# Performance work log

Measured on AMD Instinct MI355X. Metric: run time of the kernel, lower is better.

The kernel has to match this reference:

```python
import jax, jax.numpy as jnp
import numpy as np

B, L, E, H = 2, 2048, 1024, 16
D = E // H  # head dim = 64


def setup_inputs() -> dict:
    key = jax.random.key(0)
    ks = jax.random.split(key, 10)
    s = 0.02
    return {
        "xt": jax.random.normal(ks[0], (B, L, E), jnp.float32),
        "xs": jax.random.normal(ks[1], (B, L, E), jnp.float32),
        "Wt": jax.random.normal(ks[2], (E, 3 * E), jnp.float32) * s,  # t_attn weight (x @ Wt)
        "bt": jnp.zeros((3 * E,), jnp.float32),
        "Ws": jax.random.normal(ks[3], (E, 2 * E), jnp.float32) * s,  # s_attn weight
        "bs": jnp.zeros((2 * E,), jnp.float32),
        "Wc": jax.random.normal(ks[4], (E, E), jnp.float32) * s,      # c_proj weight
        "bc": jnp.zeros((E,), jnp.float32),
        "lam_ts": jnp.ones((1,), jnp.float32),
        "lam_st": jnp.ones((1,), jnp.float32),
        "lam_ss": jnp.ones((1,), jnp.float32),
    }


def _heads(x):
    # (B, L, E) -> (B, H, L, D)
    return x.reshape(B, L, H, D).transpose(0, 2, 1, 3)


def reference(xt, xs, Wt, bt, Ws, bs, Wc, bc, lam_ts, lam_st, lam_ss):
    qt, kt, vt = jnp.split(xt @ Wt + bt, 3, axis=2)
    qs, ks = jnp.split(xs @ Ws + bs, 2, axis=2)
    qt, kt, vt, qs, ks = map(_heads, (qt, kt, vt, qs, ks))

    # 4-way disentangled scores; fuse the 4 matmuls into 2 by combining keys:
    # qt@kt^T + lam_ts*qt@ks^T = qt @ (kt + lam_ts*ks)^T
    # lam_st*qs@kt^T + lam_ss*qs@ks^T = qs @ (lam_st*kt + lam_ss*ks)^T
    k1 = kt + lam_ts[0] * ks
    k2 = lam_st[0] * kt + lam_ss[0] * ks
    att = (jnp.einsum('bhqd,bhkd->bhqk', qt, k1)
           + jnp.einsum('bhqd,bhkd->bhqk', qs, k2)) * (1.0 / np.sqrt(D))
    att = jax.nn.softmax(att, axis=-1)
    y = jnp.einsum('bhqk,bhkd->bhqd', att, vt)  # (B, H, L, D)
    y = y.transpose(0, 2, 1, 3).reshape(B, L, E)
    return y @ Wc + bc
```

## Files before the change

### kernel.cpp

```cpp
#include <hip/hip_runtime.h>
#include <math.h>

#define LQ 2048
#define EQ 1024
#define M_ROWS 4096
#define BH 32

typedef _Float16 f16x8 __attribute__((ext_vector_type(8)));
typedef _Float16 f16x4 __attribute__((ext_vector_type(4)));
typedef _Float16 f16x2 __attribute__((ext_vector_type(2)));
typedef float f32x4 __attribute__((ext_vector_type(4)));
typedef float f32x16 __attribute__((ext_vector_type(16)));

#define QSCALE 0.1803368801111204f
#define DEFER_THR 8.0f

__device__ __forceinline__ void async_ld16(const _Float16* g, _Float16* l) {
  __builtin_amdgcn_global_load_lds(
      (const __attribute__((address_space(1))) unsigned int*)g,
      (__attribute__((address_space(3))) unsigned int*)l, 16, 0, 0);
}

__global__ __launch_bounds__(256) void prep(
    const float* __restrict__ xt, const float* __restrict__ xs,
    const float* __restrict__ Wt, const float* __restrict__ Ws,
    const float* __restrict__ Wc,
    _Float16* __restrict__ xt16, _Float16* __restrict__ xs16,
    _Float16* __restrict__ WtT, _Float16* __restrict__ WsT,
    _Float16* __restrict__ WcT) {
  int gb = blockIdx.x;
  if (gb < 4096) {
    int i = gb * 256 + threadIdx.x;
    const float* s; _Float16* d; size_t off;
    if (i < 524288) { s = xt; d = xt16; off = (size_t)i * 8; }
    else            { s = xs; d = xs16; off = (size_t)(i - 524288) * 8; }
    float4 a = *(const float4*)&s[off];
    float4 b = *(const float4*)&s[off + 4];
    f16x8 h;
    h[0] = (_Float16)a.x; h[1] = (_Float16)a.y; h[2] = (_Float16)a.z; h[3] = (_Float16)a.w;
    h[4] = (_Float16)b.x; h[5] = (_Float16)b.y; h[6] = (_Float16)b.z; h[7] = (_Float16)b.w;
    *(f16x8*)&d[off] = h;
  } else {
    __shared__ float T[32][65];
    int tb = gb - 4096;
    int c0 = (tb % 96) * 64;
    int k0 = (tb / 96) * 32;
    const float* W; _Float16* D; int Nw, cl;
    if (c0 < 3072)      { W = Wt; D = WtT; Nw = 3072; cl = c0; }
    else if (c0 < 5120) { W = Ws; D = WsT; Nw = 2048; cl = c0 - 3072; }
    else                { W = Wc; D = WcT; Nw = 1024; cl = c0 - 5120; }
    const int tid = threadIdx.x;
#pragma unroll
    for (int p = 0; p < 4; ++p) {
      int idx = tid + p * 256;
      int row = idx >> 5;
      int c2 = (idx & 31) * 2;
      float2 v = *(const float2*)&W[(size_t)(k0 + row) * Nw + cl + c2];
      T[row][c2] = v.x;
      T[row][c2 + 1] = v.y;
    }
    __syncthreads();
#pragma unroll
    for (int p = 0; p < 4; ++p) {
      int idx = tid + p * 256;
      int col = idx >> 4;
      int k2 = (idx & 15) * 2;
      f16x2 h2;
      h2[0] = (_Float16)T[k2][col];
      h2[1] = (_Float16)T[k2 + 1][col];
      *(f16x2*)&D[(size_t)(cl + col) * 1024 + k0 + k2] = h2;
    }
  }
}

__global__ __launch_bounds__(256, 3) void proj_gemm(
    const _Float16* __restrict__ xt16, const _Float16* __restrict__ xs16,
    const _Float16* __restrict__ WtT, const _Float16* __restrict__ WsT,
    const float* __restrict__ bt, const float* __restrict__ bs,
    _Float16* __restrict__ q16, _Float16* __restrict__ k16,
    _Float16* __restrict__ v16) {
  __shared__ _Float16 LS[128 * 128];
  _Float16* Al0 = LS;
  _Float16* Bl0 = LS + 4096;
  _Float16* Al1 = LS + 8192;
  _Float16* Bl1 = LS + 12288;

  const int tid = threadIdx.x;
  const int w = tid >> 6;
  const int lane = tid & 63;
  const int quad = lane >> 4;
  const int l15 = lane & 15;
  const int wm = w >> 1, wn = w & 1;

  const int wg = blockIdx.y * 16 + blockIdx.x;
  const int swz = (wg & 7) * 160 + (wg >> 3);
  const int bx = swz & 15;
  const int by = swz >> 4;
  const int n0 = bx * 128;

  const _Float16* Ab;
  const _Float16* Bb;
  const float* bias;
  int m0, bsel = 0, branch;
  if (by < 32) {
    branch = 0; Ab = xt16; Bb = WtT; bias = bt; m0 = by * 128;
  } else if (by < 48) {
    branch = 1;
    int by2 = by - 32;
    bsel = by2 >> 3;
    m0 = (by2 & 7) * 128;
    Ab = WtT + (size_t)2048 * 1024;
    Bb = xt16 + (size_t)bsel * 2048 * 1024;
    bias = bt;
  } else {
    branch = 2; Ab = xs16; Bb = WsT; bias = bs; m0 = (by - 48) * 128;
  }

  const int srow = lane >> 2;
  const int schunk = ((lane & 3) ^ ((lane >> 3) & 3)) * 8;
  const int key = (l15 >> 1) & 3;

  f32x4 acc[4][4];
#pragma unroll
  for (int mb = 0; mb < 4; ++mb)
#pragma unroll
    for (int nb = 0; nb < 4; ++nb) acc[mb][nb] = (f32x4){0.f, 0.f, 0.f, 0.f};

  auto dma = [&](int kt, _Float16* Al, _Float16* Bl) {
#pragma unroll
    for (int i = 0; i < 2; ++i) {
      int rt = w * 32 + i * 16;
      async_ld16(&Ab[(size_t)(m0 + rt + srow) * 1024 + kt + schunk], &Al[rt * 32]);
      async_ld16(&Bb[(size_t)(n0 + rt + srow) * 1024 + kt + schunk], &Bl[rt * 32]);
    }
  };

  auto comp = [&](const _Float16* Al, const _Float16* Bl) {
    f16x8 af[4], bf[4];
    const int pc = (quad ^ key) * 8;
#pragma unroll
    for (int mb = 0; mb < 4; ++mb)
      af[mb] = *(const f16x8*)&Al[(wm * 64 + mb * 16 + l15) * 32 + pc];
#pragma unroll
    for (int nb = 0; nb < 4; ++nb)
      bf[nb] = *(const f16x8*)&Bl[(wn * 64 + nb * 16 + l15) * 32 + pc];
#pragma unroll
    for (int mb = 0; mb < 4; ++mb)
#pragma unroll
      for (int nb = 0; nb < 4; ++nb)
        acc[mb][nb] = __builtin_amdgcn_mfma_f32_16x16x32_f16(bf[nb], af[mb], acc[mb][nb], 0, 0, 0);
  };

  dma(0, Al0, Bl0);
  for (int kt = 0; kt < 1024; kt += 64) {
    __syncthreads();
    dma(kt + 32, Al1, Bl1);
    comp(Al0, Bl0);
    __syncthreads();
    if (kt + 64 < 1024) dma(kt + 64, Al0, Bl0);
    comp(Al1, Bl1);
  }

  __syncthreads();
#pragma unroll
  for (int mb = 0; mb < 4; ++mb) {
    const int rowL = wm * 64 + mb * 16 + l15;
    const int rx = (rowL & 7) << 3;
    float rbias = 0.f;
    if (branch == 1) rbias = bias[2048 + m0 + rowL];
#pragma unroll
    for (int nb = 0; nb < 4; ++nb) {
      const int colL = wn * 64 + nb * 16 + quad * 4;
      f16x4 o4;
      if (branch == 1) {
#pragma unroll
        for (int r = 0; r < 4; ++r) o4[r] = (_Float16)(acc[mb][nb][r] + rbias);
      } else {
        const float4 bv4 = *(const float4*)&bias[n0 + colL];
        o4[0] = (_Float16)(acc[mb][nb][0] + bv4.x);
        o4[1] = (_Float16)(acc[mb][nb][1] + bv4.y);
        o4[2] = (_Float16)(acc[mb][nb][2] + bv4.z);
        o4[3] = (_Float16)(acc[mb][nb][3] + bv4.w);
      }
      *(f16x4*)&LS[rowL * 128 + (colL ^ rx)] = o4;
    }
  }
  __syncthreads();

  const int g = tid & 15;
  const int c8 = g * 8;
#pragma unroll
  for (int p = 0; p < 8; ++p) {
    const int r = p * 16 + (tid >> 4);
    f16x8 v8 = *(const f16x8*)&LS[r * 128 + (c8 ^ ((r & 7) << 3))];
    if (branch == 1) {
      *(f16x8*)&v16[(size_t)(bsel * 1024 + m0 + r) * 2048 + n0 + c8] = v8;
    } else {
      const int grow = m0 + r;
      const int col = n0 + c8;
      const int bb = grow >> 11, ll = grow & 2047;
      const int which = col >> 10, e = col & 1023;
      const int hh = e >> 6, dd = e & 63;
      _Float16* dst = which ? k16 : q16;
      const int off = (branch == 0) ? 0 : 64;
      *(f16x8*)&dst[((size_t)(bb * 16 + hh) * 2048 + ll) * 128 + off + dd] = v8;
    }
  }
}

__global__ __launch_bounds__(256, 3) void cproj_gemm(
    const _Float16* __restrict__ A, const _Float16* __restrict__ Bm,
    const float* __restrict__ bias, float* __restrict__ outf) {
  __shared__ _Float16 Al0[128 * 32];
  __shared__ _Float16 Bl0[64 * 32];
  __shared__ _Float16 Al1[128 * 32];
  __shared__ _Float16 Bl1[64 * 32];

  const int tid = threadIdx.x;
  const int w = tid >> 6;
  const int lane = tid & 63;
  const int quad = lane >> 4;
  const int l15 = lane & 15;
  const int wm = w >> 1, wn = w & 1;
  const int m0 = blockIdx.y * 128;
  const int n0 = blockIdx.x * 64;

  const int srow = lane >> 2;
  const int schunk = ((lane & 3) ^ ((lane >> 3) & 3)) * 8;

  f32x4 acc[4][2];
#pragma unroll
  for (int mb = 0; mb < 4; ++mb)
#pragma unroll
    for (int nb = 0; nb < 2; ++nb) acc[mb][nb] = (f32x4){0.f, 0.f, 0.f, 0.f};

  const int key = (l15 >> 1) & 3;

  auto dma = [&](int kt, _Float16* Al, _Float16* Bl) {
#pragma unroll
    for (int i = 0; i < 2; ++i) {
      int rt = w * 32 + i * 16;
      async_ld16(&A[(size_t)(m0 + rt + srow) * 1024 + kt + schunk], &Al[rt * 32]);
    }
    int rtb = w * 16;
    async_ld16(&Bm[(size_t)(n0 + rtb + srow) * 1024 + kt + schunk], &Bl[rtb * 32]);
  };

  auto comp = [&](const _Float16* Al, const _Float16* Bl) {
    f16x8 af[4], bf[2];
    const int pc = (quad ^ key) * 8;
#pragma unroll
    for (int mb = 0; mb < 4; ++mb)
      af[mb] = *(const f16x8*)&Al[(wm * 64 + mb * 16 + l15) * 32 + pc];
#pragma unroll
    for (int nb = 0; nb < 2; ++nb)
      bf[nb] = *(const f16x8*)&Bl[(wn * 32 + nb * 16 + l15) * 32 + pc];
#pragma unroll
    for (int mb = 0; mb < 4; ++mb)
#pragma unroll
      for (int nb = 0; nb < 2; ++nb)
        acc[mb][nb] = __builtin_amdgcn_mfma_f32_16x16x32_f16(bf[nb], af[mb], acc[mb][nb], 0, 0, 0);
  };

  dma(0, Al0, Bl0);
  for (int kt = 0; kt < 1024; kt += 64) {
    __syncthreads();
    dma(kt + 32, Al1, Bl1);
    comp(Al0, Bl0);
    __syncthreads();
    if (kt + 64 < 1024) dma(kt + 64, Al0, Bl0);
    comp(Al1, Bl1);
  }

#pragma unroll
  for (int nb = 0; nb < 2; ++nb) {
    const int col0 = n0 + wn * 32 + nb * 16 + quad * 4;
    const float4 bv4 = *(const float4*)&bias[col0];
#pragma unroll
    for (int mb = 0; mb < 4; ++mb) {
      int row = m0 + wm * 64 + mb * 16 + l15;
      float4 o4;
      o4.x = acc[mb][nb][0] + bv4.x;
      o4.y = acc[mb][nb][1] + bv4.y;
      o4.z = acc[mb][nb][2] + bv4.z;
      o4.w = acc[mb][nb][3] + bv4.w;
      *(float4*)&outf[(size_t)row * 1024 + col0] = o4;
    }
  }
}

__global__ __launch_bounds__(256, 2) void flash_attn_mfma(
    const _Float16* __restrict__ qcat, const _Float16* __restrict__ kcat,
    const _Float16* __restrict__ vT, _Float16* __restrict__ y,
    const float* __restrict__ lam_ts, const float* __restrict__ lam_st,
    const float* __restrict__ lam_ss) {
  const int bh = blockIdx.y;
  const int qt0 = blockIdx.x * 128;
  const int b = bh >> 4, h = bh & 15;
  const _Float16* Qg = qcat + (size_t)bh * LQ * 128;
  const _Float16* Kg = kcat + (size_t)bh * LQ * 128;
  const _Float16* Vg = vT + (size_t)bh * 64 * LQ;

  __shared__ _Float16 K0s[64 * 128];
  __shared__ _Float16 K1s[64 * 128];
  __shared__ _Float16 V0s[64 * 64];
  __shared__ _Float16 V1s[64 * 64];
  __shared__ _Float16 V2s[64 * 64];
  __shared__ _Float16 V3s[64 * 64];

  const int tid = threadIdx.x;
  const int w = tid >> 6;
  const int lane = tid & 63;
  const int half = lane >> 5;
  const int l31 = lane & 31;

  const float lts = lam_ts[0], lst = lam_st[0], lss = lam_ss[0];

  f16x8 qf[8];
#pragma unroll
  for (int db = 0; db < 4; ++db) {
    const _Float16* qp = &Qg[(size_t)(qt0 + w * 32 + l31) * 128 + db * 16 + half * 8];
    f16x8 a = *(const f16x8*)qp;
    f16x8 bq = *(const f16x8*)(qp + 64);
#pragma unroll
    for (int e = 0; e < 8; ++e) {
      float fa = (float)a[e], fb = (float)bq[e];
      qf[db][e]     = (_Float16)(QSCALE * (fa + lst * fb));
      qf[db + 4][e] = (_Float16)(QSCALE * (lts * fa + lss * fb));
    }
  }

  float m_i = -INFINITY;
  float l_i = 0.f;
  f32x16 O[2];
#pragma unroll
  for (int nt = 0; nt < 2; ++nt)
#pragma unroll
    for (int r = 0; r < 16; ++r) O[nt][r] = 0.f;

  auto dma_k = [&](int t, _Float16* Kd) {
#pragma unroll
    for (int a = 0; a < 4; ++a) {
      int row = w * 16 + a * 4 + (lane >> 4);
      int sc = (lane & 15) ^ (row & 7);
      async_ld16(&Kg[(size_t)(t + row) * 128 + sc * 8], &Kd[(w * 16 + a * 4) * 128]);
    }
  };
  auto dma_v = [&](int t, _Float16* Vd) {
#pragma unroll
    for (int a = 0; a < 2; ++a) {
      int row = w * 16 + a * 8 + (lane >> 3);
      int sc = (lane & 7) ^ (row & 7);
      async_ld16(&Vg[(size_t)row * LQ + t + sc * 8], &Vd[(w * 16 + a * 8) * 64]);
    }
  };

  auto qk = [&](const _Float16* Ks, f32x16* Sp) {
#pragma unroll
    for (int kb = 0; kb < 2; ++kb)
#pragma unroll
      for (int r = 0; r < 16; ++r) Sp[kb][r] = 0.f;
#pragma unroll
    for (int db = 0; db < 8; ++db) {
      const int pc = ((db * 2 + half) ^ (lane & 7)) * 8;
      f16x8 af0 = *(const f16x8*)&Ks[l31 * 128 + pc];
      f16x8 af1 = *(const f16x8*)&Ks[(32 + l31) * 128 + pc];
      Sp[0] = __builtin_amdgcn_mfma_f32_32x32x16_f16(af0, qf[db], Sp[0], 0, 0, 0);
      Sp[1] = __builtin_amdgcn_mfma_f32_32x32x16_f16(af1, qf[db], Sp[1], 0, 0, 0);
    }
  };

  auto softpv = [&](f32x16* S, const _Float16* Vs) {
    float mx = -INFINITY;
#pragma unroll
    for (int kb = 0; kb < 2; ++kb)
#pragma unroll
      for (int r = 0; r < 16; ++r) mx = fmaxf(mx, S[kb][r]);
    mx = fmaxf(mx, __shfl_xor(mx, 32));

    if (__any(mx > m_i + DEFER_THR)) {
      float m_new = fmaxf(m_i, mx);
      float alpha = __builtin_amdgcn_exp2f(m_i - m_new);
      l_i *= alpha;
#pragma unroll
      for (int nt = 0; nt < 2; ++nt)
#pragma unroll
        for (int r = 0; r < 16; ++r) O[nt][r] *= alpha;
      m_i = m_new;
    }

    float s = 0.f;
#pragma unroll
    for (int kb = 0; kb < 2; ++kb)
#pragma unroll
      for (int r = 0; r < 16; ++r) {
        float p = __builtin_amdgcn_exp2f(S[kb][r] - m_i);
        S[kb][r] = p;
        s += p;
      }
    s += __shfl_xor(s, 32);
    l_i += s;

#pragma unroll
    for (int kb = 0; kb < 2; ++kb) {
      unsigned pu[8];
#pragma unroll
      for (int i = 0; i < 8; ++i) {
        f16x2 t2;
        t2[0] = (_Float16)S[kb][2 * i];
        t2[1] = (_Float16)S[kb][2 * i + 1];
        pu[i] = __builtin_bit_cast(unsigned, t2);
      }
#pragma unroll
      for (int c = 0; c < 2; ++c) {
        unsigned u0 = pu[4 * c + 0], u1 = pu[4 * c + 1];
        unsigned u2 = pu[4 * c + 2], u3 = pu[4 * c + 3];
        asm("v_permlane32_swap_b32 %0, %1" : "+v"(u0), "+v"(u2));
        asm("v_permlane32_swap_b32 %0, %1" : "+v"(u1), "+v"(u3));
        union { unsigned u[4]; f16x8 v; } pb;
        pb.u[0] = u0; pb.u[1] = u1; pb.u[2] = u2; pb.u[3] = u3;
        const int kb2 = kb * 2 + c;
        f16x8 av[2];
#pragma unroll
        for (int nt = 0; nt < 2; ++nt) {
          int dim = nt * 32 + l31;
          int pc = ((kb2 * 2 + half) ^ (dim & 7)) * 8;
          av[nt] = *(const f16x8*)&Vs[dim * 64 + pc];
        }
#pragma unroll
        for (int nt = 0; nt < 2; ++nt)
          O[nt] = __builtin_amdgcn_mfma_f32_32x32x16_f16(av[nt], pb.v, O[nt], 0, 0, 0);
      }
    }
  };

  f32x16 Sa[2], Sb[2];

  dma_k(0, K0s);
  dma_v(0, V0s);
  __syncthreads();
  dma_k(64, K1s);
  dma_v(64, V1s);
  qk(K0s, Sb);

  for (int j = 0; j < 7; ++j) {
    const int t = j * 256 + 64;
    __syncthreads();
    dma_k(t + 64, K0s);  dma_v(t + 64, V2s);
    qk(K1s, Sa);  softpv(Sb, V0s);
    __syncthreads();
    dma_k(t + 128, K1s); dma_v(t + 128, V3s);
    qk(K0s, Sb);  softpv(Sa, V1s);
    __syncthreads();
    dma_k(t + 192, K0s); dma_v(t + 192, V0s);
    qk(K1s, Sa);  softpv(Sb, V2s);
    __syncthreads();
    dma_k(t + 256, K1s); dma_v(t + 256, V1s);
    qk(K0s, Sb);  softpv(Sa, V3s);
  }

  __syncthreads();
  dma_k(1920, K0s); dma_v(1920, V2s);
  qk(K1s, Sa);  softpv(Sb, V0s);
  __syncthreads();
  dma_k(1984, K1s); dma_v(1984, V3s);
  qk(K0s, Sb);  softpv(Sa, V1s);
  __syncthreads();
  qk(K1s, Sa);  softpv(Sb, V2s);
  softpv(Sa, V3s);

  float inv = 1.f / l_i;
  int qrow = qt0 + w * 32 + l31;
#pragma unroll
  for (int nt = 0; nt < 2; ++nt)
#pragma unroll
    for (int rg = 0; rg < 4; ++rg) {
      f16x4 o4;
#pragma unroll
      for (int i = 0; i < 4; ++i) o4[i] = (_Float16)(O[nt][rg * 4 + i] * inv);
      int dim = nt * 32 + rg * 8 + half * 4;
      *(f16x4*)&y[((size_t)b * LQ + qrow) * EQ + h * 64 + dim] = o4;
    }
}

extern "C" void kernel_launch(void* const* d_in, const int* in_sizes, int n_in,
                              void* d_out, int out_size, void* d_ws, size_t ws_size,
                              hipStream_t stream) {
  const float* xt = (const float*)d_in[0];
  const float* xs = (const float*)d_in[1];
  const float* Wt = (const float*)d_in[2];
  const float* bt = (const float*)d_in[3];
  const float* Ws = (const float*)d_in[4];
  const float* bs = (const float*)d_in[5];
  const float* Wc = (const float*)d_in[6];
  const float* bc = (const float*)d_in[7];
  const float* lam_ts = (const float*)d_in[8];
  const float* lam_st = (const float*)d_in[9];
  const float* lam_ss = (const float*)d_in[10];
  float* out = (float*)d_out;

  _Float16* w16 = (_Float16*)d_ws;
  _Float16* xt16 = w16;
  _Float16* xs16 = xt16 + 4194304;
  _Float16* WtT  = xs16 + 4194304;
  _Float16* WsT  = WtT + 3145728;
  _Float16* WcT  = WsT + 2097152;
  _Float16* qcat = WcT + 1048576;
  _Float16* kcat = qcat + 8388608;
  _Float16* vbufT = kcat + 8388608;
  _Float16* ybuf = vbufT + 4194304;

  prep<<<7168, 256, 0, stream>>>(xt, xs, Wt, Ws, Wc, xt16, xs16, WtT, WsT, WcT);
  proj_gemm<<<dim3(16, 80), 256, 0, stream>>>(
      xt16, xs16, WtT, WsT, bt, bs, qcat, kcat, vbufT);
  flash_attn_mfma<<<dim3(16, 32), 256, 0, stream>>>(
      qcat, kcat, vbufT, ybuf, lam_ts, lam_st, lam_ss);
  cproj_gemm<<<dim3(16, 32), 256, 0, stream>>>(ybuf, WcT, bc, out);
}
```

Baseline: 254.6 us.

## Halve flash attention query and KV tiles, use two-wave blocks

Shrinks the attention block from 4 waves and 128 queries to 2 waves and 64 queries, and the KV tile from 64 to 32 keys. The QK and PV lambdas are restructured for a single 32x32 score tile per wave, the LDS buffers and V swizzle are resized, and the grid doubles in x. The aim is more blocks for better CU load balance and lower LDS and register pressure. In exchange each K/V tile is reused by half as many queries, so global/L2 traffic and barrier count per unit of work roughly double.

```diff
diff --git a/kernel.cpp b/kernel.cpp
--- a/kernel.cpp
+++ b/kernel.cpp
@@ -289,24 +289,24 @@
   }
 }
 
-__global__ __launch_bounds__(256, 2) void flash_attn_mfma(
+__global__ __launch_bounds__(128, 2) void flash_attn_mfma(
     const _Float16* __restrict__ qcat, const _Float16* __restrict__ kcat,
     const _Float16* __restrict__ vT, _Float16* __restrict__ y,
     const float* __restrict__ lam_ts, const float* __restrict__ lam_st,
     const float* __restrict__ lam_ss) {
   const int bh = blockIdx.y;
-  const int qt0 = blockIdx.x * 128;
+  const int qt0 = blockIdx.x * 64;
   const int b = bh >> 4, h = bh & 15;
   const _Float16* Qg = qcat + (size_t)bh * LQ * 128;
   const _Float16* Kg = kcat + (size_t)bh * LQ * 128;
   const _Float16* Vg = vT + (size_t)bh * 64 * LQ;
 
-  __shared__ _Float16 K0s[64 * 128];
-  __shared__ _Float16 K1s[64 * 128];
-  __shared__ _Float16 V0s[64 * 64];
-  __shared__ _Float16 V1s[64 * 64];
-  __shared__ _Float16 V2s[64 * 64];
-  __shared__ _Float16 V3s[64 * 64];
+  __shared__ _Float16 K0s[32 * 128];
+  __shared__ _Float16 K1s[32 * 128];
+  __shared__ _Float16 V0s[64 * 32];
+  __shared__ _Float16 V1s[64 * 32];
+  __shared__ _Float16 V2s[64 * 32];
+  __shared__ _Float16 V3s[64 * 32];
 
   const int tid = threadIdx.x;
   const int w = tid >> 6;
@@ -349,33 +349,28 @@
   auto dma_v = [&](int t, _Float16* Vd) {
 #pragma unroll
     for (int a = 0; a < 2; ++a) {
-      int row = w * 16 + a * 8 + (lane >> 3);
-      int sc = (lane & 7) ^ (row & 7);
-      async_ld16(&Vg[(size_t)row * LQ + t + sc * 8], &Vd[(w * 16 + a * 8) * 64]);
+      int row = w * 32 + a * 16 + (lane >> 2);
+      int sc = (lane & 3) ^ (row & 3);
+      async_ld16(&Vg[(size_t)row * LQ + t + sc * 8], &Vd[(w * 32 + a * 16) * 32]);
     }
   };
 
   auto qk = [&](const _Float16* Ks, f32x16* Sp) {
 #pragma unroll
-    for (int kb = 0; kb < 2; ++kb)
-#pragma unroll
-      for (int r = 0; r < 16; ++r) Sp[kb][r] = 0.f;
+    for (int r = 0; r < 16; ++r) (*Sp)[r] = 0.f;
 #pragma unroll
     for (int db = 0; db < 8; ++db) {
       const int pc = ((db * 2 + half) ^ (lane & 7)) * 8;
       f16x8 af0 = *(const f16x8*)&Ks[l31 * 128 + pc];
-      f16x8 af1 = *(const f16x8*)&Ks[(32 + l31) * 128 + pc];
-      Sp[0] = __builtin_amdgcn_mfma_f32_32x32x16_f16(af0, qf[db], Sp[0], 0, 0, 0);
-      Sp[1] = __builtin_amdgcn_mfma_f32_32x32x16_f16(af1, qf[db], Sp[1], 0, 0, 0);
-    }
-  };
-
-  auto softpv = [&](f32x16* S, const _Float16* Vs) {
+      *Sp = __builtin_amdgcn_mfma_f32_32x32x16_f16(af0, qf[db], *Sp, 0, 0, 0);
+    }
+  };
+
+  auto softpv = [&](f32x16* Sp, const _Float16* Vs) {
+    f32x16& S = *Sp;
     float mx = -INFINITY;
 #pragma unroll
-    for (int kb = 0; kb < 2; ++kb)
-#pragma unroll
-      for (int r = 0; r < 16; ++r) mx = fmaxf(mx, S[kb][r]);
+    for (int r = 0; r < 16; ++r) mx = fmaxf(mx, S[r]);
     mx = fmaxf(mx, __shfl_xor(mx, 32));
 
     if (__any(mx > m_i + DEFER_THR)) {
@@ -391,83 +386,77 @@
 
     float s = 0.f;
 #pragma unroll
-    for (int kb = 0; kb < 2; ++kb)
-#pragma unroll
-      for (int r = 0; r < 16; ++r) {
-        float p = __builtin_amdgcn_exp2f(S[kb][r] - m_i);
-        S[kb][r] = p;
-        s += p;
-      }
+    for (int r = 0; r < 16; ++r) {
+      float p = __builtin_amdgcn_exp2f(S[r] - m_i);
+      S[r] = p;
+      s += p;
+    }
     s += __shfl_xor(s, 32);
     l_i += s;
 
-#pragma unroll
-    for (int kb = 0; kb < 2; ++kb) {
-      unsigned pu[8];
-#pragma unroll
-      for (int i = 0; i < 8; ++i) {
-        f16x2 t2;
-        t2[0] = (_Float16)S[kb][2 * i];
-        t2[1] = (_Float16)S[kb][2 * i + 1];
-        pu[i] = __builtin_bit_cast(unsigned, t2);
+    unsigned pu[8];
+#pragma unroll
+    for (int i = 0; i < 8; ++i) {
+      f16x2 t2;
+      t2[0] = (_Float16)S[2 * i];
+      t2[1] = (_Float16)S[2 * i + 1];
+      pu[i] = __builtin_bit_cast(unsigned, t2);
+    }
+#pragma unroll
+    for (int c = 0; c < 2; ++c) {
+      unsigned u0 = pu[4 * c + 0], u1 = pu[4 * c + 1];
+      unsigned u2 = pu[4 * c + 2], u3 = pu[4 * c + 3];
+      asm("v_permlane32_swap_b32 %0, %1" : "+v"(u0), "+v"(u2));
+      asm("v_permlane32_swap_b32 %0, %1" : "+v"(u1), "+v"(u3));
+      union { unsigned u[4]; f16x8 v; } pb;
+      pb.u[0] = u0; pb.u[1] = u1; pb.u[2] = u2; pb.u[3] = u3;
+      f16x8 av[2];
+#pragma unroll
+      for (int nt = 0; nt < 2; ++nt) {
+        int dim = nt * 32 + l31;
+        int pc = ((c * 2 + half) ^ (dim & 3)) * 8;
+        av[nt] = *(const f16x8*)&Vs[dim * 32 + pc];
       }
 #pragma unroll
-      for (int c = 0; c < 2; ++c) {
-        unsigned u0 = pu[4 * c + 0], u1 = pu[4 * c + 1];
-        unsigned u2 = pu[4 * c + 2], u3 = pu[4 * c + 3];
-        asm("v_permlane32_swap_b32 %0, %1" : "+v"(u0), "+v"(u2));
-        asm("v_permlane32_swap_b32 %0, %1" : "+v"(u1), "+v"(u3));
-        union { unsigned u[4]; f16x8 v; } pb;
-        pb.u[0] = u0; pb.u[1] = u1; pb.u[2] = u2; pb.u[3] = u3;
-        const int kb2 = kb * 2 + c;
-        f16x8 av[2];
-#pragma unroll
-        for (int nt = 0; nt < 2; ++nt) {
-          int dim = nt * 32 + l31;
-          int pc = ((kb2 * 2 + half) ^ (dim & 7)) * 8;
-          av[nt] = *(const f16x8*)&Vs[dim * 64 + pc];
-        }
-#pragma unroll
-        for (int nt = 0; nt < 2; ++nt)
-          O[nt] = __builtin_amdgcn_mfma_f32_32x32x16_f16(av[nt], pb.v, O[nt], 0, 0, 0);
-      }
-    }
-  };
-
-  f32x16 Sa[2], Sb[2];
+      for (int nt = 0; nt < 2; ++nt)
+        O[nt] = __builtin_amdgcn_mfma_f32_32x32x16_f16(av[nt], pb.v, O[nt], 0, 0, 0);
+    }
+  };
+
+  f32x16 Sa, Sb;
 
   dma_k(0, K0s);
   dma_v(0, V0s);
   __syncthreads();
-  dma_k(64, K1s);
-  dma_v(64, V1s);
-  qk(K0s, Sb);
-
-  for (int j = 0; j < 7; ++j) {
-    const int t = j * 256 + 64;
-    __syncthreads();
-    dma_k(t + 64, K0s);  dma_v(t + 64, V2s);
-    qk(K1s, Sa);  softpv(Sb, V0s);
-    __syncthreads();
-    dma_k(t + 128, K1s); dma_v(t + 128, V3s);
-    qk(K0s, Sb);  softpv(Sa, V1s);
-    __syncthreads();
-    dma_k(t + 192, K0s); dma_v(t + 192, V0s);
-    qk(K1s, Sa);  softpv(Sb, V2s);
-    __syncthreads();
-    dma_k(t + 256, K1s); dma_v(t + 256, V1s);
-    qk(K0s, Sb);  softpv(Sa, V3s);
+  dma_k(32, K1s);
+  dma_v(32, V1s);
+  qk(K0s, &Sb);
+
+  for (int j = 0; j < 15; ++j) {
+    const int t = j * 128 + 32;
+    __syncthreads();
+    dma_k(t + 32, K0s);  dma_v(t + 32, V2s);
+    qk(K1s, &Sa);  softpv(&Sb, V0s);
+    __syncthreads();
+    dma_k(t + 64, K1s);  dma_v(t + 64, V3s);
+    qk(K0s, &Sb);  softpv(&Sa, V1s);
+    __syncthreads();
+    dma_k(t + 96, K0s);  dma_v(t + 96, V0s);
+    qk(K1s, &Sa);  softpv(&Sb, V2s);
+    __syncthreads();
+    dma_k(t + 128, K1s); dma_v(t + 128, V1s);
+    qk(K0s, &Sb);  softpv(&Sa, V3s);
   }
 
   __syncthreads();
-  dma_k(1920, K0s); dma_v(1920, V2s);
-  qk(K1s, Sa);  softpv(Sb, V0s);
+  dma_k(1984, K0s); dma_v(1984, V2s);
+  qk(K1s, &Sa);  softpv(&Sb, V0s);
   __syncthreads();
-  dma_k(1984, K1s); dma_v(1984, V3s);
-  qk(K0s, Sb);  softpv(Sa, V1s);
+  dma_k(2016, K1s); dma_v(2016, V3s);
+  qk(K0s, &Sb);  softpv(&Sa, V1s);
   __syncthreads();
-  qk(K1s, Sa);  softpv(Sb, V2s);
-  softpv(Sa, V3s);
+  qk(K1s, &Sa);  softpv(&Sb, V2s);
+  softpv(&Sa, V3s);
 
   float inv = 1.f / l_i;
   int qrow = qt0 + w * 32 + l31;
@@ -513,7 +502,7 @@
   prep<<<7168, 256, 0, stream>>>(xt, xs, Wt, Ws, Wc, xt16, xs16, WtT, WsT, WcT);
   proj_gemm<<<dim3(16, 80), 256, 0, stream>>>(
       xt16, xs16, WtT, WsT, bt, bs, qcat, kcat, vbufT);
-  flash_attn_mfma<<<dim3(16, 32), 256, 0, stream>>>(
+  flash_attn_mfma<<<dim3(32, 32), 128, 0, stream>>>(
       qcat, kcat, vbufT, ybuf, lam_ts, lam_st, lam_ss);
   cproj_gemm<<<dim3(16, 32), 256, 0, stream>>>(ybuf, WcT, bc, out);
 }
```

Result: slower. 266.2 us (+4.6%).
